# Optimization experiments

Measured on AMD Instinct MI355X. Metric: run time of the kernel, lower is better.

The kernel has to match this reference:

```python
import jax, jax.numpy as jnp
import numpy as np

QMIN, QMAX = -128, 127  # int8 range

def setup_inputs() -> dict:
    key = jax.random.key(0)
    k1, k2, k3 = jax.random.split(key, 3)
    B, S, DIN, DOUT = 8, 2048, 4096, 4096
    x = jax.random.normal(k1, (B, S, DIN), dtype=jnp.float32)
    weight = jax.random.normal(k2, (DOUT, DIN), dtype=jnp.float32) * 0.02
    bias = jax.random.normal(k3, (DOUT,), dtype=jnp.float32) * 0.01
    # per-tensor asymmetric activation qparams (as produced by a calibrated observer)
    act_scale = jnp.float32(0.05)
    act_zero_point = jnp.int32(3)
    # per-output-channel symmetric weight scales (block_size = (1, in_features))
    weight_scale = jnp.max(jnp.abs(weight), axis=1) / 127.0  # [DOUT]
    return {"x": x, "weight": weight, "bias": bias,
            "act_scale": act_scale, "act_zero_point": act_zero_point,
            "weight_scale": weight_scale}

def reference(x, weight, bias, act_scale, act_zero_point, weight_scale):
    # 1) quantize activations: per-tensor asymmetric int8
    qx = jnp.clip(jnp.round(x / act_scale) + act_zero_point, QMIN, QMAX).astype(jnp.int8)
    # 2) quantize weight: per-output-channel symmetric int8 (zero_point = 0)
    qw = jnp.clip(jnp.round(weight / weight_scale[:, None]), QMIN, QMAX).astype(jnp.int8)
    acc = jnp.einsum('bsk,nk->bsn',
                     qx.astype(jnp.int32) - act_zero_point.astype(jnp.int32),
                     qw.astype(jnp.int32))  # [B, S, DOUT] int32
    # 4) dequantize: combined scale = act_scale * weight_scale[n], then bias
    out = acc.astype(jnp.float32) * (act_scale * weight_scale) + bias
    return out
```

## Files before the change

### kernel.cpp

```cpp
#include <hip/hip_runtime.h>
#include <cstdint>

#define M_DIM 16384
#define N_DIM 4096
#define K_DIM 4096

#define BM 128
#define BN 128
#define BK 64

typedef __attribute__((ext_vector_type(4))) int int32x4;

#define GLLD16(g, l)                                              \
  __builtin_amdgcn_global_load_lds(                               \
      (const __attribute__((address_space(1))) void*)(g),         \
      (__attribute__((address_space(3))) void*)(l), 16, 0, 0)

__global__ void quant_x_kernel(const float* __restrict__ x,
                               const float* __restrict__ sp,
                               const int* __restrict__ zpp,
                               int8_t* __restrict__ qx) {
  const float s = sp[0];
  const int zp = zpp[0];
  const long long t = (long long)blockIdx.x * blockDim.x + threadIdx.x;
  const float4* x4 = (const float4*)x;
  unsigned packed[4];
#pragma unroll
  for (int i = 0; i < 4; i++) {
    float4 v = x4[t * 4 + i];
    int q0 = min(127, max(-128, (int)rintf(v.x / s) + zp));
    int q1 = min(127, max(-128, (int)rintf(v.y / s) + zp));
    int q2 = min(127, max(-128, (int)rintf(v.z / s) + zp));
    int q3 = min(127, max(-128, (int)rintf(v.w / s) + zp));
    packed[i] = (unsigned)(q0 & 255) | ((unsigned)(q1 & 255) << 8) |
                ((unsigned)(q2 & 255) << 16) | ((unsigned)(q3 & 255) << 24);
  }
  int4 outv;
  outv.x = (int)packed[0]; outv.y = (int)packed[1];
  outv.z = (int)packed[2]; outv.w = (int)packed[3];
  ((int4*)qx)[t] = outv;
}

__global__ void quant_w_kernel(const float* __restrict__ w,
                               const float* __restrict__ wscale,
                               const float* __restrict__ bias,
                               const float* __restrict__ sp,
                               const int* __restrict__ zpp,
                               int8_t* __restrict__ qw,
                               float* __restrict__ cs,
                               float* __restrict__ off) {
  const int n = blockIdx.x;
  const float ws = wscale[n];
  const float s = sp[0];
  const int zp = zpp[0];
  const float4* wr = (const float4*)(w + (size_t)n * K_DIM);
  unsigned* qr = (unsigned*)(qw + (size_t)n * K_DIM);
  int sum = 0;
#pragma unroll
  for (int it = 0; it < K_DIM / (256 * 4); it++) {
    const int idx = it * 256 + threadIdx.x;
    float4 v = wr[idx];
    int q0 = min(127, max(-128, (int)rintf(v.x / ws)));
    int q1 = min(127, max(-128, (int)rintf(v.y / ws)));
    int q2 = min(127, max(-128, (int)rintf(v.z / ws)));
    int q3 = min(127, max(-128, (int)rintf(v.w / ws)));
    sum += q0 + q1 + q2 + q3;
    qr[idx] = (unsigned)(q0 & 255) | ((unsigned)(q1 & 255) << 8) |
              ((unsigned)(q2 & 255) << 16) | ((unsigned)(q3 & 255) << 24);
  }
  __shared__ int red[4];
#pragma unroll
  for (int o = 32; o > 0; o >>= 1) sum += __shfl_down(sum, o, 64);
  if ((threadIdx.x & 63) == 0) red[threadIdx.x >> 6] = sum;
  __syncthreads();
  if (threadIdx.x == 0) {
    const int tot = red[0] + red[1] + red[2] + red[3];
    const float c = s * ws;
    cs[n] = c;
    off[n] = bias[n] - (float)(zp * tot) * c;
  }
}

__global__ __launch_bounds__(256) void gemm_i8(
    const int8_t* __restrict__ qx, const int8_t* __restrict__ qw,
    const float* __restrict__ cs, const float* __restrict__ off,
    float* __restrict__ out) {
  __shared__ __align__(16) int8_t As[BM * BK];
  __shared__ __align__(16) int8_t Bs[BN * BK];

  const int tid = threadIdx.x;
  const int lane = tid & 63;
  const int wave = tid >> 6;
  const int wm = wave >> 1;
  const int wn = wave & 1;

  const int n0 = blockIdx.x * BN;
  const int m0 = blockIdx.y * BM;

  int32x4 acc[4][4] = {};

  const int ci = wave * 2;
  const int sr0 = (ci + 0) * 16 + (lane >> 2);
  const int sr1 = (ci + 1) * 16 + (lane >> 2);
  const int sc0 = (lane & 3) ^ ((sr0 >> 1) & 3);
  const int sc1 = (lane & 3) ^ ((sr1 >> 1) & 3);

  const int8_t* gA0 = qx + (size_t)(m0 + sr0) * K_DIM + sc0 * 16;
  const int8_t* gA1 = qx + (size_t)(m0 + sr1) * K_DIM + sc1 * 16;
  const int8_t* gB0 = qw + (size_t)(n0 + sr0) * K_DIM + sc0 * 16;
  const int8_t* gB1 = qw + (size_t)(n0 + sr1) * K_DIM + sc1 * 16;

  int8_t* ldsA0 = As + (ci + 0) * 1024;
  int8_t* ldsA1 = As + (ci + 1) * 1024;
  int8_t* ldsB0 = Bs + (ci + 0) * 1024;
  int8_t* ldsB1 = Bs + (ci + 1) * 1024;

  const int fr = lane & 15;
  const int quad = lane >> 4;
  const int fch = (quad ^ ((fr >> 1) & 3)) * 16;

  int aoff[4], boff[4];
#pragma unroll
  for (int t = 0; t < 4; t++) {
    aoff[t] = (wm * 64 + t * 16 + fr) * BK + fch;
    boff[t] = (wn * 64 + t * 16 + fr) * BK + fch;
  }

  for (int kt = 0; kt < K_DIM; kt += BK) {
    __syncthreads();
    GLLD16(gA0 + kt, ldsA0);
    GLLD16(gA1 + kt, ldsA1);
    GLLD16(gB0 + kt, ldsB0);
    GLLD16(gB1 + kt, ldsB1);
    __syncthreads();

    int32x4 af[4], bf[4];
#pragma unroll
    for (int t = 0; t < 4; t++) {
      af[t] = *(const int32x4*)(As + aoff[t]);
      bf[t] = *(const int32x4*)(Bs + boff[t]);
    }
#pragma unroll
    for (int tm = 0; tm < 4; tm++)
#pragma unroll
      for (int tn = 0; tn < 4; tn++)
        acc[tm][tn] = __builtin_amdgcn_mfma_i32_16x16x64_i8(
            af[tm], bf[tn], acc[tm][tn], 0, 0, 0);
  }

#pragma unroll
  for (int tn = 0; tn < 4; tn++) {
    const int col = n0 + wn * 64 + tn * 16 + fr;
    const float c = cs[col];
    const float o = off[col];
#pragma unroll
    for (int tm = 0; tm < 4; tm++) {
      const int rowb = m0 + wm * 64 + tm * 16 + quad * 4;
#pragma unroll
      for (int r = 0; r < 4; r++) {
        out[(size_t)(rowb + r) * N_DIM + col] = (float)acc[tm][tn][r] * c + o;
      }
    }
  }
}

extern "C" void kernel_launch(void* const* d_in, const int* in_sizes, int n_in,
                              void* d_out, int out_size, void* d_ws,
                              size_t ws_size, hipStream_t stream) {
  const float* x = (const float*)d_in[0];
  const float* w = (const float*)d_in[1];
  const float* bias = (const float*)d_in[2];
  const float* act_scale = (const float*)d_in[3];
  const int* zp = (const int*)d_in[4];
  const float* wscale = (const float*)d_in[5];
  float* out = (float*)d_out;

  int8_t* qx = (int8_t*)d_ws;
  int8_t* qw = qx + (size_t)M_DIM * K_DIM;
  float* cs = (float*)(qw + (size_t)N_DIM * K_DIM);
  float* off = cs + N_DIM;

  quant_x_kernel<<<16384, 256, 0, stream>>>(x, act_scale, zp, qx);
  quant_w_kernel<<<N_DIM, 256, 0, stream>>>(w, wscale, bias, act_scale, zp,
                                            qw, cs, off);
  gemm_i8<<<dim3(N_DIM / BN, M_DIM / BM), 256, 0, stream>>>(qx, qw, cs, off,
                                                            out);
}
```

Before: 792.4 us.

## Rewrite int8 GEMM as 256x256 double-buffered pipelined kernel with 8 waves

Grows the GEMM tile to 256x256x128 with 512 threads and a 128 KB LDS double buffer. Global-to-LDS loads for later k-steps are interleaved with MFMA phases under explicit vmcnt/lgkmcnt waits, barriers and setprio, so memory latency is hidden and operand reuse per byte loaded goes up. It also adds a block-index swizzle for L2 locality, and the activation quant kernel now writes coalesced 4-byte stores. The risks are lower occupancy, since the large LDS allocation sits badly with launch_bounds(512,2), and subtle hazards in the hand-written wait counts.

```diff
diff --git a/kernel.cpp b/kernel.cpp
--- a/kernel.cpp
+++ b/kernel.cpp
@@ -5,9 +5,9 @@
 #define N_DIM 4096
 #define K_DIM 4096
 
-#define BM 128
-#define BN 128
-#define BK 64
+#define BM 256
+#define BN 256
+#define BK 128
 
 typedef __attribute__((ext_vector_type(4))) int int32x4;
 
@@ -22,23 +22,20 @@
                                int8_t* __restrict__ qx) {
   const float s = sp[0];
   const int zp = zpp[0];
-  const long long t = (long long)blockIdx.x * blockDim.x + threadIdx.x;
+  const size_t b = (size_t)blockIdx.x * 1024;
   const float4* x4 = (const float4*)x;
-  unsigned packed[4];
+  unsigned* q4 = (unsigned*)qx;
 #pragma unroll
   for (int i = 0; i < 4; i++) {
-    float4 v = x4[t * 4 + i];
+    const size_t idx = b + (size_t)i * 256 + threadIdx.x;
+    float4 v = x4[idx];
     int q0 = min(127, max(-128, (int)rintf(v.x / s) + zp));
     int q1 = min(127, max(-128, (int)rintf(v.y / s) + zp));
     int q2 = min(127, max(-128, (int)rintf(v.z / s) + zp));
     int q3 = min(127, max(-128, (int)rintf(v.w / s) + zp));
-    packed[i] = (unsigned)(q0 & 255) | ((unsigned)(q1 & 255) << 8) |
-                ((unsigned)(q2 & 255) << 16) | ((unsigned)(q3 & 255) << 24);
-  }
-  int4 outv;
-  outv.x = (int)packed[0]; outv.y = (int)packed[1];
-  outv.z = (int)packed[2]; outv.w = (int)packed[3];
-  ((int4*)qx)[t] = outv;
+    q4[idx] = (unsigned)(q0 & 255) | ((unsigned)(q1 & 255) << 8) |
+              ((unsigned)(q2 & 255) << 16) | ((unsigned)(q3 & 255) << 24);
+  }
 }
 
 __global__ void quant_w_kernel(const float* __restrict__ w,
@@ -81,87 +78,162 @@
   }
 }
 
-__global__ __launch_bounds__(256) void gemm_i8(
+__global__ __launch_bounds__(512, 2) void gemm_i8(
     const int8_t* __restrict__ qx, const int8_t* __restrict__ qw,
     const float* __restrict__ cs, const float* __restrict__ off,
     float* __restrict__ out) {
-  __shared__ __align__(16) int8_t As[BM * BK];
-  __shared__ __align__(16) int8_t Bs[BN * BK];
+  __shared__ __align__(16) int8_t lds[131072];
 
   const int tid = threadIdx.x;
   const int lane = tid & 63;
   const int wave = tid >> 6;
-  const int wm = wave >> 1;
-  const int wn = wave & 1;
-
-  const int n0 = blockIdx.x * BN;
-  const int m0 = blockIdx.y * BM;
-
-  int32x4 acc[4][4] = {};
-
-  const int ci = wave * 2;
-  const int sr0 = (ci + 0) * 16 + (lane >> 2);
-  const int sr1 = (ci + 1) * 16 + (lane >> 2);
-  const int sc0 = (lane & 3) ^ ((sr0 >> 1) & 3);
-  const int sc1 = (lane & 3) ^ ((sr1 >> 1) & 3);
-
-  const int8_t* gA0 = qx + (size_t)(m0 + sr0) * K_DIM + sc0 * 16;
-  const int8_t* gA1 = qx + (size_t)(m0 + sr1) * K_DIM + sc1 * 16;
-  const int8_t* gB0 = qw + (size_t)(n0 + sr0) * K_DIM + sc0 * 16;
-  const int8_t* gB1 = qw + (size_t)(n0 + sr1) * K_DIM + sc1 * 16;
-
-  int8_t* ldsA0 = As + (ci + 0) * 1024;
-  int8_t* ldsA1 = As + (ci + 1) * 1024;
-  int8_t* ldsB0 = Bs + (ci + 0) * 1024;
-  int8_t* ldsB1 = Bs + (ci + 1) * 1024;
+  const int wm = wave >> 2;
+  const int wn = wave & 3;
+
+  const int bid = blockIdx.x;
+  const int swz = (bid & 7) * 128 + (bid >> 3);
+  const int n0 = (swz & 15) * BN;
+  const int m0 = (swz >> 4) * BM;
+
+  int32x4 acc[8][4] = {};
+  int32x4 af[8], bf0[4], bf1[4];
+
+  const int scol = ((lane & 7) ^ ((lane >> 3) & 7)) * 16;
+  const int8_t* pA[2][2];
+  const int8_t* pB[2][2];
+#pragma unroll
+  for (int h = 0; h < 2; h++)
+#pragma unroll
+    for (int j = 0; j < 2; j++) {
+      const int r = h * 128 + (wave * 2 + j) * 8 + (lane >> 3);
+      const int ga = ((r >> 6) & 1) * 128 + (r >> 7) * 64 + (r & 63);
+      const int gb = ((r >> 5) & 3) * 64 + (r >> 7) * 32 + (r & 31);
+      pA[h][j] = qx + (size_t)(m0 + ga) * K_DIM + scol;
+      pB[h][j] = qw + (size_t)(n0 + gb) * K_DIM + scol;
+    }
 
   const int fr = lane & 15;
   const int quad = lane >> 4;
-  const int fch = (quad ^ ((fr >> 1) & 3)) * 16;
-
-  int aoff[4], boff[4];
-#pragma unroll
-  for (int t = 0; t < 4; t++) {
-    aoff[t] = (wm * 64 + t * 16 + fr) * BK + fch;
-    boff[t] = (wn * 64 + t * 16 + fr) * BK + fch;
-  }
-
-  for (int kt = 0; kt < K_DIM; kt += BK) {
-    __syncthreads();
-    GLLD16(gA0 + kt, ldsA0);
-    GLLD16(gA1 + kt, ldsA1);
-    GLLD16(gB0 + kt, ldsB0);
-    GLLD16(gB1 + kt, ldsB1);
-    __syncthreads();
-
-    int32x4 af[4], bf[4];
-#pragma unroll
-    for (int t = 0; t < 4; t++) {
-      af[t] = *(const int32x4*)(As + aoff[t]);
-      bf[t] = *(const int32x4*)(Bs + boff[t]);
-    }
-#pragma unroll
-    for (int tm = 0; tm < 4; tm++)
-#pragma unroll
-      for (int tn = 0; tn < 4; tn++)
-        acc[tm][tn] = __builtin_amdgcn_mfma_i32_16x16x64_i8(
-            af[tm], bf[tn], acc[tm][tn], 0, 0, 0);
-  }
-
-#pragma unroll
-  for (int tn = 0; tn < 4; tn++) {
-    const int col = n0 + wn * 64 + tn * 16 + fr;
+  int aoffs[8], boffs[4];
+#pragma unroll
+  for (int mtl = 0; mtl < 4; mtl++)
+#pragma unroll
+    for (int ks = 0; ks < 2; ks++) {
+      const int r = wm * 64 + mtl * 16 + fr;
+      const int c = (ks * 4 + quad) ^ (fr & 7);
+      aoffs[mtl * 2 + ks] = r * 128 + c * 16;
+    }
+#pragma unroll
+  for (int ntl = 0; ntl < 2; ntl++)
+#pragma unroll
+    for (int ks = 0; ks < 2; ks++) {
+      const int r = wn * 32 + ntl * 16 + fr;
+      const int c = (ks * 4 + quad) ^ (fr & 7);
+      boffs[ntl * 2 + ks] = r * 128 + c * 16;
+    }
+
+#define STAGE(rbase, h, P, kb)                                          \
+  do {                                                                  \
+    GLLD16(P[h][0] + (kb), lds + (rbase) + (h) * 16384 + wave * 2048);  \
+    GLLD16(P[h][1] + (kb),                                              \
+           lds + (rbase) + (h) * 16384 + wave * 2048 + 1024);           \
+  } while (0)
+
+#define LDA(buf, h)                                                     \
+  do {                                                                  \
+    _Pragma("unroll") for (int q = 0; q < 8; q++) af[q] =               \
+        *(const int32x4*)(lds + (buf) * 65536 + (h) * 16384 + aoffs[q]); \
+  } while (0)
+
+#define LDB(buf, g, BF)                                                 \
+  do {                                                                  \
+    _Pragma("unroll") for (int q = 0; q < 4; q++) BF[q] =               \
+        *(const int32x4*)(lds + (buf) * 65536 + 32768 + (g) * 16384 +   \
+                          boffs[q]);                                    \
+  } while (0)
+
+#define MM(h, g, BF)                                                       \
+  do {                                                                    \
+    _Pragma("unroll") for (int mtl = 0; mtl < 4; mtl++)                   \
+        _Pragma("unroll") for (int ntl = 0; ntl < 2; ntl++) {             \
+      acc[(h)*4 + mtl][(g)*2 + ntl] = __builtin_amdgcn_mfma_i32_16x16x64_i8( \
+          af[mtl * 2 + 0], BF[ntl * 2 + 0], acc[(h)*4 + mtl][(g)*2 + ntl], \
+          0, 0, 0);                                                        \
+      acc[(h)*4 + mtl][(g)*2 + ntl] = __builtin_amdgcn_mfma_i32_16x16x64_i8( \
+          af[mtl * 2 + 1], BF[ntl * 2 + 1], acc[(h)*4 + mtl][(g)*2 + ntl], \
+          0, 0, 0);                                                        \
+    }                                                                      \
+  } while (0)
+
+#define BAR() __builtin_amdgcn_s_barrier()
+#define WAITLGKM() asm volatile("s_waitcnt lgkmcnt(0)" ::: "memory")
+#define VM6() asm volatile("s_waitcnt vmcnt(6)" ::: "memory")
+#define PRIO(x) __builtin_amdgcn_s_setprio(x)
+
+  STAGE(0, 0, pA, 0);
+  STAGE(0, 1, pA, 0);
+  STAGE(32768, 0, pB, 0);
+  STAGE(32768, 1, pB, 0);
+  STAGE(65536, 0, pA, 128);
+  STAGE(98304, 0, pB, 128);
+  STAGE(98304, 1, pB, 128);
+  VM6();
+  BAR();
+
+  for (int i = 0; i < K_DIM / (2 * BK); i++) {
+    const int kb1 = ((2 * i + 1) << 7) & (K_DIM - 1);
+    const int kb2 = ((2 * i + 2) << 7) & (K_DIM - 1);
+    const int kb3 = ((2 * i + 3) << 7) & (K_DIM - 1);
+    LDA(0, 0);
+    LDB(0, 0, bf0);
+    STAGE(65536, 1, pA, kb1);
+    BAR(); WAITLGKM(); PRIO(1); MM(0, 0, bf0); PRIO(0); BAR();
+    LDB(0, 1, bf1);
+    STAGE(0, 0, pA, kb2);
+    BAR(); WAITLGKM(); PRIO(1); MM(0, 1, bf1); PRIO(0); BAR();
+    LDA(0, 1);
+    STAGE(32768, 0, pB, kb2);
+    BAR(); WAITLGKM(); PRIO(1); MM(1, 1, bf1); PRIO(0); BAR();
+    STAGE(32768, 1, pB, kb2);
+    VM6();
+    BAR(); PRIO(1); MM(1, 0, bf0); PRIO(0); BAR();
+    LDA(1, 0);
+    LDB(1, 0, bf0);
+    STAGE(0, 1, pA, kb2);
+    BAR(); WAITLGKM(); PRIO(1); MM(0, 0, bf0); PRIO(0); BAR();
+    LDB(1, 1, bf1);
+    STAGE(65536, 0, pA, kb3);
+    BAR(); WAITLGKM(); PRIO(1); MM(0, 1, bf1); PRIO(0); BAR();
+    LDA(1, 1);
+    STAGE(98304, 0, pB, kb3);
+    BAR(); WAITLGKM(); PRIO(1); MM(1, 1, bf1); PRIO(0); BAR();
+    STAGE(98304, 1, pB, kb3);
+    VM6();
+    BAR(); PRIO(1); MM(1, 0, bf0); PRIO(0); BAR();
+  }
+
+#pragma unroll
+  for (int nt = 0; nt < 4; nt++) {
+    const int col = n0 + wn * 64 + nt * 16 + fr;
     const float c = cs[col];
     const float o = off[col];
 #pragma unroll
-    for (int tm = 0; tm < 4; tm++) {
-      const int rowb = m0 + wm * 64 + tm * 16 + quad * 4;
+    for (int mt = 0; mt < 8; mt++) {
+      const int rowb = m0 + wm * 128 + mt * 16 + quad * 4;
 #pragma unroll
       for (int r = 0; r < 4; r++) {
-        out[(size_t)(rowb + r) * N_DIM + col] = (float)acc[tm][tn][r] * c + o;
+        out[(size_t)(rowb + r) * N_DIM + col] = (float)acc[mt][nt][r] * c + o;
       }
     }
   }
+#undef STAGE
+#undef LDA
+#undef LDB
+#undef MM
+#undef BAR
+#undef WAITLGKM
+#undef VM6
+#undef PRIO
 }
 
 extern "C" void kernel_launch(void* const* d_in, const int* in_sizes, int n_in,
@@ -183,6 +255,6 @@
   quant_x_kernel<<<16384, 256, 0, stream>>>(x, act_scale, zp, qx);
   quant_w_kernel<<<N_DIM, 256, 0, stream>>>(w, wscale, bias, act_scale, zp,
                                             qw, cs, off);
-  gemm_i8<<<dim3(N_DIM / BN, M_DIM / BM), 256, 0, stream>>>(qx, qw, cs, off,
-                                                            out);
-}
+  gemm_i8<<<dim3((M_DIM / BM) * (N_DIM / BN)), 512, 0, stream>>>(qx, qw, cs,
+                                                                 off, out);
+}
```

New measurement: 703.4 us. 11.2% less time.
